# Performance work log

Measured on AMD Instinct MI355X. Metric: run time of the kernel, lower is better.

The kernel has to match this reference:

```python
import jax, jax.numpy as jnp
import numpy as np

HIDDEN = 2048
N_HEADS = 32
N_KV_HEADS = 8
HEAD_DIM = HIDDEN // N_HEADS  # 64
N_REP = N_HEADS // N_KV_HEADS  # 4
ROPE_THETA = 10000.0


def setup_inputs() -> dict:
    key = jax.random.key(0)
    ks = jax.random.split(key, 6)
    B, S = 1, 2048
    scale = 0.02
    return {
        "hidden_states": jax.random.normal(ks[0], (B, S, HIDDEN), dtype=jnp.float32),
        "Wq": jax.random.normal(ks[1], (HIDDEN, N_HEADS * HEAD_DIM), dtype=jnp.float32) * scale,
        "Wk": jax.random.normal(ks[2], (HIDDEN, N_KV_HEADS * HEAD_DIM), dtype=jnp.float32) * scale,
        "Wv": jax.random.normal(ks[3], (HIDDEN, N_KV_HEADS * HEAD_DIM), dtype=jnp.float32) * scale,
        "Wo": jax.random.normal(ks[4], (HIDDEN, HIDDEN), dtype=jnp.float32) * scale,
        "position_ids": jnp.arange(S, dtype=jnp.int64 if jax.config.jax_enable_x64 else jnp.int32)[None, :],
    }


def _rope_cos_sin(position_ids, dtype):
    # inv_freq: [head_dim//2]
    inv_freq = 1.0 / (ROPE_THETA ** (jnp.arange(0, HEAD_DIM, 2, dtype=jnp.float32) / HEAD_DIM))
    # freqs: [B, S, head_dim//2]
    freqs = position_ids.astype(jnp.float32)[:, :, None] * inv_freq[None, None, :]
    emb = jnp.concatenate([freqs, freqs], axis=-1)  # [B, S, head_dim]
    return jnp.cos(emb).astype(dtype), jnp.sin(emb).astype(dtype)


def _rotate_half(x):
    x1, x2 = jnp.split(x, 2, axis=-1)
    return jnp.concatenate([-x2, x1], axis=-1)


def reference(hidden_states, Wq, Wk, Wv, Wo, position_ids):
    B, S, _ = hidden_states.shape
    # projections -> [B, H, S, D]
    q = (hidden_states @ Wq).reshape(B, S, N_HEADS, HEAD_DIM).transpose(0, 2, 1, 3)
    k = (hidden_states @ Wk).reshape(B, S, N_KV_HEADS, HEAD_DIM).transpose(0, 2, 1, 3)
    v = (hidden_states @ Wv).reshape(B, S, N_KV_HEADS, HEAD_DIM).transpose(0, 2, 1, 3)

    cos, sin = _rope_cos_sin(position_ids, hidden_states.dtype)
    cos = cos[:, None, :, :]  # [B,1,S,D]
    sin = sin[:, None, :, :]
    q = q * cos + _rotate_half(q) * sin
    k = k * cos + _rotate_half(k) * sin

    # GQA: expand kv heads
    k = jnp.repeat(k, N_REP, axis=1)  # [B, H, S, D]
    v = jnp.repeat(v, N_REP, axis=1)

    scores = jnp.einsum("bhqd,bhkd->bhqk", q, k) / np.sqrt(HEAD_DIM).astype(np.float32)
    # additive causal mask
    causal = jnp.tril(jnp.ones((S, S), dtype=bool))
    scores = jnp.where(causal[None, None, :, :], scores, jnp.finfo(jnp.float32).min)
    attn = jax.nn.softmax(scores.astype(jnp.float32), axis=-1).astype(q.dtype)

    out = jnp.einsum("bhqk,bhkd->bhqd", attn, v)  # [B,H,S,D]
    out = out.transpose(0, 2, 1, 3).reshape(B, S, HIDDEN)
    return out @ Wo
```

## Files before the change

### kernel.cpp

```cpp
#include <hip/hip_runtime.h>
#include <stdint.h>

typedef __attribute__((ext_vector_type(8))) short short8;
typedef __attribute__((ext_vector_type(4))) float floatx4;
typedef __attribute__((ext_vector_type(16))) float floatx16;

__device__ __forceinline__ float b2f(unsigned short u) {
    union { unsigned int i; float f; } x; x.i = ((unsigned int)u) << 16; return x.f;
}
__device__ __forceinline__ unsigned short f2b(float f) {
    unsigned int x = __float_as_uint(f);
    return (unsigned short)((x + 0x7FFFu + ((x >> 16) & 1u)) >> 16);
}
__device__ __forceinline__ unsigned int cvt_pk_bf16(float lo, float hi) {
    unsigned int r;
    asm("v_cvt_pk_bf16_f32 %0, %1, %2" : "=v"(r) : "v"(lo), "v"(hi));
    return r;
}
__device__ __forceinline__ float exp2_(float x) {
    float r;
    asm("v_exp_f32 %0, %1" : "=v"(r) : "v"(x));
    return r;
}

__device__ __forceinline__ void gload_lds16(const void* g, void* l) {
    __builtin_amdgcn_global_load_lds((const __attribute__((address_space(1))) unsigned int*)g,
                                     (__attribute__((address_space(3))) unsigned int*)l, 16, 0, 0);
}

__global__ __launch_bounds__(256)
void prep_kernel(const float* __restrict__ Wq, const float* __restrict__ Wk,
                 const float* __restrict__ Wv, const float* __restrict__ Wo,
                 const float* __restrict__ hs,
                 unsigned short* __restrict__ Wqkv, unsigned short* __restrict__ WoT,
                 unsigned short* __restrict__ hs_b) {
    __shared__ float tile[64][65];
    int b = blockIdx.x;
    if (b >= 2560) {
        int i = ((b - 2560) * 256 + threadIdx.x) * 4;
        float4 v = *reinterpret_cast<const float4*>(hs + i);
        hs_b[i + 0] = f2b(v.x);
        hs_b[i + 1] = f2b(v.y);
        hs_b[i + 2] = f2b(v.z);
        hs_b[i + 3] = f2b(v.w);
        return;
    }
    const float* in;
    unsigned short* out;
    int bx, by, ld_in, ld_out;
    if (b < 1024) {
        in = Wq; out = Wqkv; bx = b & 31; by = b >> 5; ld_in = 2048; ld_out = 2048;
    } else if (b < 1280) {
        int c = b - 1024;
        in = Wk; out = Wqkv + (size_t)2048 * 2048; bx = c & 7; by = c >> 3; ld_in = 512; ld_out = 2048;
    } else if (b < 1536) {
        int c = b - 1280;
        in = Wv; out = Wqkv + (size_t)2560 * 2048; bx = c & 7; by = c >> 3; ld_in = 512; ld_out = 2048;
    } else {
        int c = b - 1536;
        in = Wo; out = WoT; bx = c & 31; by = c >> 5; ld_in = 2048; ld_out = 2048;
    }
    int tx = threadIdx.x & 63, ty = threadIdx.x >> 6;
    int c0 = bx * 64, r0 = by * 64;
    #pragma unroll
    for (int i = 0; i < 64; i += 4)
        tile[ty + i][tx] = in[(size_t)(r0 + ty + i) * ld_in + c0 + tx];
    __syncthreads();
    #pragma unroll
    for (int i = 0; i < 64; i += 4)
        out[(size_t)(c0 + ty + i) * ld_out + r0 + tx] = f2b(tile[tx][ty + i]);
}

template<int MODE>
__global__ __launch_bounds__(256)
void gemm64x128(const unsigned short* __restrict__ A, const unsigned short* __restrict__ BT,
                void* __restrict__ Cout, unsigned short* __restrict__ vTout,
                int M, int N, int K) {
    __shared__ __align__(16) unsigned short As[2][64 * 64];
    __shared__ __align__(16) unsigned short Bs[2][128 * 64];
    int tid = threadIdx.x;
    int l = tid & 63, w = tid >> 6;
    int lr = l & 15, lg = l >> 4;

    int gx = gridDim.x;
    int nwg = gx * gridDim.y;
    int flat = blockIdx.y * gx + blockIdx.x;
    int q8 = nwg >> 3;
    int f2 = (flat & 7) * q8 + (flat >> 3);
    int bx = f2 % gx, by = f2 / gx;
    int nb = bx * 128, mb = by * 64;

    floatx4 acc[4][2];
    #pragma unroll
    for (int m = 0; m < 4; ++m)
        #pragma unroll
        for (int f = 0; f < 2; ++f) acc[m][f] = (floatx4)(0.f);

    int ca1 = tid + 256;
    int ra0 = tid >> 3, ja0 = (tid & 7) ^ (ra0 & 7);
    int ra1 = ca1 >> 3, ja1 = (ca1 & 7) ^ (ra1 & 7);
    const unsigned short* Ag0 = A + (size_t)(mb + ra0) * K + ja0 * 8;
    const unsigned short* Ag1 = A + (size_t)(mb + ra1) * K + ja1 * 8;
    const unsigned short* Bg[4];
    #pragma unroll
    for (int i = 0; i < 4; ++i) {
        int c = tid + 256 * i;
        int r = c >> 3, j = (c & 7) ^ (r & 7);
        Bg[i] = BT + (size_t)(nb + r) * K + j * 8;
    }

    auto stage = [&](int buf, int kb) {
        gload_lds16(Ag0 + kb, &As[buf][tid * 8]);
        gload_lds16(Ag1 + kb, &As[buf][ca1 * 8]);
        #pragma unroll
        for (int i = 0; i < 4; ++i)
            gload_lds16(Bg[i] + kb, &Bs[buf][(tid + 256 * i) * 8]);
    };

    int nsteps = K >> 6;
    stage(0, 0);
    for (int it = 0; it < nsteps; ++it) {
        int nxt = (it + 1 < nsteps) ? it + 1 : it;
        stage((it + 1) & 1, nxt * 64);
        asm volatile("s_waitcnt vmcnt(6)" ::: "memory");
        __builtin_amdgcn_s_barrier();
        __builtin_amdgcn_sched_barrier(0);

        const unsigned short* Ab = As[it & 1];
        const unsigned short* Bb = Bs[it & 1];
        #pragma unroll
        for (int kh = 0; kh < 2; ++kh) {
            int sl = ((kh * 4 + lg) ^ (lr & 7)) * 8;
            short8 af[4], bf[2];
            #pragma unroll
            for (int m = 0; m < 4; ++m)
                af[m] = *reinterpret_cast<const short8*>(Ab + (m * 16 + lr) * 64 + sl);
            #pragma unroll
            for (int f = 0; f < 2; ++f)
                bf[f] = *reinterpret_cast<const short8*>(Bb + (w * 32 + f * 16 + lr) * 64 + sl);
            #pragma unroll
            for (int m = 0; m < 4; ++m)
                #pragma unroll
                for (int f = 0; f < 2; ++f)
                    acc[m][f] = __builtin_amdgcn_mfma_f32_16x16x32_bf16(af[m], bf[f], acc[m][f], 0, 0, 0);
        }
        __builtin_amdgcn_sched_barrier(0);
        __builtin_amdgcn_s_barrier();
    }
    asm volatile("s_waitcnt vmcnt(0)" ::: "memory");

    #pragma unroll
    for (int m = 0; m < 4; ++m) {
        int orow = mb + m * 16 + lg * 4;
        #pragma unroll
        for (int f = 0; f < 2; ++f) {
            int ocol = nb + w * 32 + f * 16 + lr;
            if (MODE == 2 && ocol >= 2560) {
                int d = ocol - 2560;
                int kvh2 = d >> 6, dd = d & 63, dh = dd >> 5, lq2 = dd & 31;
                int t64 = orow >> 6, so = orow & 63;
                int w2 = so >> 5, so32 = so & 31, kc = so32 >> 4, so16 = so32 & 15;
                int hl2 = so16 >> 3, e0 = so16 & 7;
                size_t addr = ((size_t)((kvh2 * 32 + t64) * 8) + w2 * 4 + dh * 2 + kc) * 512
                            + (hl2 * 32 + lq2) * 8 + e0;
                unsigned long long pk =
                    (unsigned long long)cvt_pk_bf16(acc[m][f][0], acc[m][f][1])
                  | ((unsigned long long)cvt_pk_bf16(acc[m][f][2], acc[m][f][3]) << 32);
                *reinterpret_cast<unsigned long long*>(vTout + addr) = pk;
            } else {
                #pragma unroll
                for (int r = 0; r < 4; ++r) {
                    if (MODE == 1)
                        ((float*)Cout)[(size_t)(orow + r) * N + ocol] = acc[m][f][r];
                    else
                        ((unsigned short*)Cout)[(size_t)(orow + r) * N + ocol] = f2b(acc[m][f][r]);
                }
            }
        }
    }
}

__global__ void rope_kernel(unsigned short* __restrict__ qkv, unsigned short* __restrict__ kB,
                            const int* __restrict__ pos_ids) {
    int idx = blockIdx.x * blockDim.x + threadIdx.x;
    int i = idx & 31;
    int hh = (idx >> 5) % 40;
    int s = idx / 1280;
    float pos = (float)pos_ids[s];
    float inv = exp2f(-0.41524101186092029f * (float)i);
    float a = pos * inv;
    float sn, cs;
    __sincosf(a, &sn, &cs);
    if (hh < 32) {
        unsigned short* p = qkv + (size_t)s * 3072 + hh * 64;
        float x1 = b2f(p[i]), x2 = b2f(p[i + 32]);
        const float scale = 0.18033688011112042f;
        p[i]      = f2b((x1 * cs - x2 * sn) * scale);
        p[i + 32] = f2b((x2 * cs + x1 * sn) * scale);
    } else {
        int kvh = hh - 32;
        const unsigned short* p = qkv + (size_t)s * 3072 + 2048 + kvh * 64;
        float x1 = b2f(p[i]), x2 = b2f(p[i + 32]);
        float r1 = x1 * cs - x2 * sn;
        float r2 = x2 * cs + x1 * sn;
        int t32 = s >> 5, lq = s & 31;
        int dc = i >> 4, hl = (i >> 3) & 1, e = i & 7;
        size_t base = (((size_t)(kvh * 64 + t32) * 4) * 64 + hl * 32 + lq) * 8 + e;
        kB[base + (size_t)dc * 512]       = f2b(r1);
        kB[base + (size_t)(dc + 2) * 512] = f2b(r2);
    }
}

__global__ __launch_bounds__(128, 2)
void attn_kernel(const unsigned short* __restrict__ QKV,
                 const unsigned short* __restrict__ KB,
                 const unsigned short* __restrict__ VB,
                 unsigned short* __restrict__ O) {
    const int LDQ = 3072, HID = 2048;
    __shared__ float Ms[64 * 36];

    int tid = threadIdx.x;
    int l = tid & 63, w = tid >> 6;
    int lq = l & 31, hl = l >> 5;
    int b = blockIdx.x;
    int h = b & 31;
    int band = 63 - (b >> 5);
    int nT = (band >> 1) + 1;
    int kvh = h >> 2;
    int qrow = band * 32 + lq;

    short8 qf[4];
    {
        const unsigned short* Qr = QKV + (size_t)qrow * LDQ + h * 64;
        #pragma unroll
        for (int c = 0; c < 4; ++c)
            qf[c] = *reinterpret_cast<const short8*>(Qr + c * 16 + hl * 8);
    }

    const unsigned short* Kp = KB + ((size_t)(kvh * 64 + w) * 4) * 512 + l * 8;
    const size_t KSTEP = 2 * 4 * 512;
    const unsigned short* Vbase = VB + ((size_t)kvh * 32 * 8 + (size_t)w * 4) * 512 + l * 8;

    floatx16 acc[2];
    acc[0] = (floatx16)(0.f); acc[1] = (floatx16)(0.f);
    float m_run = -1e30f, l_run = 0.f;

    auto process = [&](const short8* kf, int c0w, bool diag,
                       short8 v00, short8 v01, short8 v10, short8 v11) {
        floatx16 st = (floatx16)(0.f);
        __builtin_amdgcn_s_setprio(1);
        #pragma unroll
        for (int dc = 0; dc < 4; ++dc)
            st = __builtin_amdgcn_mfma_f32_32x32x16_bf16(kf[dc], qf[dc], st, 0, 0, 0);
        __builtin_amdgcn_s_setprio(0);
        if (diag) {
            #pragma unroll
            for (int r = 0; r < 16; ++r) {
                int key = c0w + (r & 3) + 8 * (r >> 2) + 4 * hl;
                if (key > qrow) st[r] = -1e30f;
            }
        }
        float t0 = fmaxf(fmaxf(st[0], st[1]), fmaxf(st[2], st[3]));
        float t1 = fmaxf(fmaxf(st[4], st[5]), fmaxf(st[6], st[7]));
        float t2 = fmaxf(fmaxf(st[8], st[9]), fmaxf(st[10], st[11]));
        float t3 = fmaxf(fmaxf(st[12], st[13]), fmaxf(st[14], st[15]));
        float tm = fmaxf(fmaxf(t0, t1), fmaxf(t2, t3));
        tm = fmaxf(tm, __shfl_xor(tm, 32));
        if (!__all(tm <= m_run + 11.5f)) {
            float mn = fmaxf(m_run, tm);
            float al = exp2_(m_run - mn);
            l_run *= al;
            acc[0] *= al;
            acc[1] *= al;
            m_run = mn;
        }
        float p[16];
        #pragma unroll
        for (int r = 0; r < 16; ++r) p[r] = exp2_(st[r] - m_run);
        float s0 = (p[0] + p[1]) + (p[2] + p[3]);
        float s1 = (p[4] + p[5]) + (p[6] + p[7]);
        float s2 = (p[8] + p[9]) + (p[10] + p[11]);
        float s3 = (p[12] + p[13]) + (p[14] + p[15]);
        float rs = (s0 + s1) + (s2 + s3);
        rs += __shfl_xor(rs, 32);
        l_run += rs;
        unsigned int u[4][2];
        #pragma unroll
        for (int B2 = 0; B2 < 4; ++B2) {
            u[B2][0] = cvt_pk_bf16(p[B2 * 4 + 0], p[B2 * 4 + 1]);
            u[B2][1] = cvt_pk_bf16(p[B2 * 4 + 2], p[B2 * 4 + 3]);
        }
        asm volatile("s_waitcnt vmcnt(4)" ::: "memory");
        __builtin_amdgcn_sched_barrier(0);
        #pragma unroll
        for (int kc = 0; kc < 2; ++kc) {
            unsigned int o0 = u[2 * kc][0],     o1 = u[2 * kc][1];
            unsigned int e0 = u[2 * kc + 1][0], e1 = u[2 * kc + 1][1];
            unsigned int t0x = (unsigned int)__shfl((int)o0, l ^ 32);
            unsigned int t1x = (unsigned int)__shfl((int)o1, l ^ 32);
            unsigned int s0p = (unsigned int)__shfl((int)e0, l ^ 32);
            unsigned int s1p = (unsigned int)__shfl((int)e1, l ^ 32);
            union { unsigned int uu[4]; short8 s8; } pf;
            pf.uu[0] = hl ? s0p : o0;
            pf.uu[1] = hl ? s1p : o1;
            pf.uu[2] = hl ? e0 : t0x;
            pf.uu[3] = hl ? e1 : t1x;
            __builtin_amdgcn_s_setprio(1);
            acc[0] = __builtin_amdgcn_mfma_f32_32x32x16_bf16(kc ? v01 : v00, pf.s8, acc[0], 0, 0, 0);
            acc[1] = __builtin_amdgcn_mfma_f32_32x32x16_bf16(kc ? v11 : v10, pf.s8, acc[1], 0, 0, 0);
            __builtin_amdgcn_s_setprio(0);
        }
    };

    short8 kA[4], kBr[4];
    #pragma unroll
    for (int dc = 0; dc < 4; ++dc)
        kA[dc] = *reinterpret_cast<const short8*>(Kp + dc * 512);

    int j = 0;
    while (true) {
        {
            bool last = (j == nT - 1);
            const unsigned short* Vs = Vbase + (size_t)j * 8 * 512;
            short8 v00 = *reinterpret_cast<const short8*>(Vs);
            short8 v01 = *reinterpret_cast<const short8*>(Vs + 512);
            short8 v10 = *reinterpret_cast<const short8*>(Vs + 1024);
            short8 v11 = *reinterpret_cast<const short8*>(Vs + 1536);
            __builtin_amdgcn_sched_barrier(0);
            const unsigned short* Kn = last ? Kp : Kp + KSTEP;
            #pragma unroll
            for (int dc = 0; dc < 4; ++dc)
                kBr[dc] = *reinterpret_cast<const short8*>(Kn + dc * 512);
            asm volatile("s_waitcnt vmcnt(8)" ::: "memory");
            __builtin_amdgcn_sched_barrier(0);
            process(kA, j * 64 + w * 32, last, v00, v01, v10, v11);
            if (last) break;
            ++j; Kp = Kn;
        }
        {
            bool last = (j == nT - 1);
            const unsigned short* Vs = Vbase + (size_t)j * 8 * 512;
            short8 v00 = *reinterpret_cast<const short8*>(Vs);
            short8 v01 = *reinterpret_cast<const short8*>(Vs + 512);
            short8 v10 = *reinterpret_cast<const short8*>(Vs + 1024);
            short8 v11 = *reinterpret_cast<const short8*>(Vs + 1536);
            __builtin_amdgcn_sched_barrier(0);
            const unsigned short* Kn = last ? Kp : Kp + KSTEP;
            #pragma unroll
            for (int dc = 0; dc < 4; ++dc)
                kA[dc] = *reinterpret_cast<const short8*>(Kn + dc * 512);
            asm volatile("s_waitcnt vmcnt(8)" ::: "memory");
            __builtin_amdgcn_sched_barrier(0);
            process(kBr, j * 64 + w * 32, last, v00, v01, v10, v11);
            if (last) break;
            ++j; Kp = Kn;
        }
    }
    asm volatile("s_waitcnt vmcnt(0)" ::: "memory");
    __syncthreads();

    if (w == 1) {
        Ms[l * 36 + 0] = m_run;
        Ms[l * 36 + 1] = l_run;
        #pragma unroll
        for (int d = 0; d < 2; ++d)
            #pragma unroll
            for (int r = 0; r < 16; ++r)
                Ms[l * 36 + 2 + d * 16 + r] = acc[d][r];
    }
    __syncthreads();
    if (w == 0) {
        float m1 = Ms[l * 36 + 0], l1 = Ms[l * 36 + 1];
        float mm = fmaxf(m_run, m1);
        float a0 = exp2_(m_run - mm), a1 = exp2_(m1 - mm);
        float inv = 1.0f / (l_run * a0 + l1 * a1);
        a0 *= inv; a1 *= inv;
        unsigned short* Op = O + (size_t)qrow * HID + h * 64 + hl * 4;
        #pragma unroll
        for (int d = 0; d < 2; ++d)
            #pragma unroll
            for (int g4 = 0; g4 < 4; ++g4) {
                float v0 = acc[d][g4 * 4 + 0] * a0 + Ms[l * 36 + 2 + d * 16 + g4 * 4 + 0] * a1;
                float v1 = acc[d][g4 * 4 + 1] * a0 + Ms[l * 36 + 2 + d * 16 + g4 * 4 + 1] * a1;
                float v2 = acc[d][g4 * 4 + 2] * a0 + Ms[l * 36 + 2 + d * 16 + g4 * 4 + 2] * a1;
                float v3 = acc[d][g4 * 4 + 3] * a0 + Ms[l * 36 + 2 + d * 16 + g4 * 4 + 3] * a1;
                unsigned long long pk = (unsigned long long)cvt_pk_bf16(v0, v1)
                                      | ((unsigned long long)cvt_pk_bf16(v2, v3) << 32);
                *reinterpret_cast<unsigned long long*>(Op + d * 32 + g4 * 8) = pk;
            }
    }
}

extern "C" void kernel_launch(void* const* d_in, const int* in_sizes, int n_in,
                              void* d_out, int out_size, void* d_ws, size_t ws_size,
                              hipStream_t stream) {
    const int S = 2048, HID = 2048, KVD = 512, NQKV = 3072;
    const float* hs = (const float*)d_in[0];
    const float* Wq = (const float*)d_in[1];
    const float* Wk = (const float*)d_in[2];
    const float* Wv = (const float*)d_in[3];
    const float* Wo = (const float*)d_in[4];
    const int* pos  = (const int*)d_in[5];

    char* base = (char*)d_ws;
    auto alloc = [&](size_t bytes) {
        char* r = base;
        base += (bytes + 255) & ~(size_t)255;
        return r;
    };
    unsigned short* hs_b     = (unsigned short*)alloc((size_t)S * HID * 2);
    unsigned short* Wqkv     = (unsigned short*)alloc((size_t)NQKV * HID * 2);
    unsigned short* WoT      = (unsigned short*)alloc((size_t)HID * HID * 2);
    unsigned short* qkv      = (unsigned short*)alloc((size_t)S * NQKV * 2);
    unsigned short* vB       = (unsigned short*)alloc((size_t)KVD * S * 2);
    unsigned short* kBuf     = (unsigned short*)alloc((size_t)KVD * S * 2);
    unsigned short* attn_out = (unsigned short*)alloc((size_t)S * HID * 2);

    prep_kernel<<<6656, 256, 0, stream>>>(Wq, Wk, Wv, Wo, hs, Wqkv, WoT, hs_b);

    gemm64x128<2><<<dim3(NQKV / 128, S / 64), 256, 0, stream>>>(hs_b, Wqkv, qkv, vB, S, NQKV, HID);

    rope_kernel<<<10240, 256, 0, stream>>>(qkv, kBuf, pos);

    attn_kernel<<<2048, 128, 0, stream>>>(qkv, kBuf, vB, attn_out);

    gemm64x128<1><<<dim3(HID / 128, S / 64), 256, 0, stream>>>(attn_out, WoT, (float*)d_out, nullptr, S, HID, HID);
}
```

Baseline: 125.8 us.

## Fuse RoPE into QKV projection GEMM epilogue via LDS exchange

Result: faster. 121.6 us, median of 2 (-3.3%).

```diff
diff --git a/kernel.cpp b/kernel.cpp
--- a/kernel.cpp
+++ b/kernel.cpp
@@ -75,6 +75,7 @@
 __global__ __launch_bounds__(256)
 void gemm64x128(const unsigned short* __restrict__ A, const unsigned short* __restrict__ BT,
                 void* __restrict__ Cout, unsigned short* __restrict__ vTout,
+                unsigned short* __restrict__ kBout, const int* __restrict__ pos_ids,
                 int M, int N, int K) {
     __shared__ __align__(16) unsigned short As[2][64 * 64];
     __shared__ __align__(16) unsigned short Bs[2][128 * 64];
@@ -149,13 +150,69 @@
     }
     asm volatile("s_waitcnt vmcnt(0)" ::: "memory");
 
+    if (MODE == 2 && nb < 2560) {
+        float* Xs = (float*)&Bs[0][0];
+        if (w & 1) {
+            float* dst = Xs + ((size_t)(w >> 1) * 64 + l) * 32;
+            #pragma unroll
+            for (int m = 0; m < 4; ++m)
+                #pragma unroll
+                for (int f = 0; f < 2; ++f)
+                    #pragma unroll
+                    for (int r = 0; r < 4; ++r)
+                        dst[m * 8 + f * 4 + r] = acc[m][f][r];
+        }
+        __syncthreads();
+        if (!(w & 1)) {
+            const float* src = Xs + ((size_t)(w >> 1) * 64 + l) * 32;
+            bool isQ = (nb < 2048);
+            float qs = isQ ? 0.18033688011112042f : 1.0f;
+            int kvh = isQ ? 0 : (((nb - 2048) >> 6) + (w >> 1));
+            #pragma unroll
+            for (int f = 0; f < 2; ++f) {
+                int i = f * 16 + lr;
+                float invf = exp2f(-0.41524101186092029f * (float)i);
+                int ocol = nb + w * 32 + f * 16 + lr;
+                #pragma unroll
+                for (int m = 0; m < 4; ++m) {
+                    int orow = mb + m * 16 + lg * 4;
+                    #pragma unroll
+                    for (int r = 0; r < 4; ++r) {
+                        int s = orow + r;
+                        float pos = (float)pos_ids[s];
+                        float sn, cs;
+                        __sincosf(pos * invf, &sn, &cs);
+                        float x1 = acc[m][f][r];
+                        float x2 = src[m * 8 + f * 4 + r];
+                        float r1 = (x1 * cs - x2 * sn) * qs;
+                        float r2 = (x2 * cs + x1 * sn) * qs;
+                        if (isQ) {
+                            unsigned short* C = (unsigned short*)Cout;
+                            C[(size_t)s * N + ocol]      = f2b(r1);
+                            C[(size_t)s * N + ocol + 32] = f2b(r2);
+                        } else {
+                            int t32 = s >> 5, lq2 = s & 31;
+                            int d1 = i, d2 = i + 32;
+                            int dc1 = d1 >> 4, hl1 = (d1 >> 3) & 1, e1 = d1 & 7;
+                            int dc2 = d2 >> 4, hl2 = (d2 >> 3) & 1, e2 = d2 & 7;
+                            size_t tb = (size_t)(kvh * 64 + t32) * 2048;
+                            kBout[tb + (size_t)dc1 * 512 + (hl1 * 32 + lq2) * 8 + e1] = f2b(r1);
+                            kBout[tb + (size_t)dc2 * 512 + (hl2 * 32 + lq2) * 8 + e2] = f2b(r2);
+                        }
+                    }
+                }
+            }
+        }
+        return;
+    }
+
     #pragma unroll
     for (int m = 0; m < 4; ++m) {
         int orow = mb + m * 16 + lg * 4;
         #pragma unroll
         for (int f = 0; f < 2; ++f) {
             int ocol = nb + w * 32 + f * 16 + lr;
-            if (MODE == 2 && ocol >= 2560) {
+            if (MODE == 2) {
                 int d = ocol - 2560;
                 int kvh2 = d >> 6, dd = d & 63, dh = dd >> 5, lq2 = dd & 31;
                 int t64 = orow >> 6, so = orow & 63;
@@ -180,37 +237,6 @@
     }
 }
 
-__global__ void rope_kernel(unsigned short* __restrict__ qkv, unsigned short* __restrict__ kB,
-                            const int* __restrict__ pos_ids) {
-    int idx = blockIdx.x * blockDim.x + threadIdx.x;
-    int i = idx & 31;
-    int hh = (idx >> 5) % 40;
-    int s = idx / 1280;
-    float pos = (float)pos_ids[s];
-    float inv = exp2f(-0.41524101186092029f * (float)i);
-    float a = pos * inv;
-    float sn, cs;
-    __sincosf(a, &sn, &cs);
-    if (hh < 32) {
-        unsigned short* p = qkv + (size_t)s * 3072 + hh * 64;
-        float x1 = b2f(p[i]), x2 = b2f(p[i + 32]);
-        const float scale = 0.18033688011112042f;
-        p[i]      = f2b((x1 * cs - x2 * sn) * scale);
-        p[i + 32] = f2b((x2 * cs + x1 * sn) * scale);
-    } else {
-        int kvh = hh - 32;
-        const unsigned short* p = qkv + (size_t)s * 3072 + 2048 + kvh * 64;
-        float x1 = b2f(p[i]), x2 = b2f(p[i + 32]);
-        float r1 = x1 * cs - x2 * sn;
-        float r2 = x2 * cs + x1 * sn;
-        int t32 = s >> 5, lq = s & 31;
-        int dc = i >> 4, hl = (i >> 3) & 1, e = i & 7;
-        size_t base = (((size_t)(kvh * 64 + t32) * 4) * 64 + hl * 32 + lq) * 8 + e;
-        kB[base + (size_t)dc * 512]       = f2b(r1);
-        kB[base + (size_t)(dc + 2) * 512] = f2b(r2);
-    }
-}
-
 __global__ __launch_bounds__(128, 2)
 void attn_kernel(const unsigned short* __restrict__ QKV,
                  const unsigned short* __restrict__ KB,
@@ -418,11 +444,9 @@
 
     prep_kernel<<<6656, 256, 0, stream>>>(Wq, Wk, Wv, Wo, hs, Wqkv, WoT, hs_b);
 
-    gemm64x128<2><<<dim3(NQKV / 128, S / 64), 256, 0, stream>>>(hs_b, Wqkv, qkv, vB, S, NQKV, HID);
-
-    rope_kernel<<<10240, 256, 0, stream>>>(qkv, kBuf, pos);
+    gemm64x128<2><<<dim3(NQKV / 128, S / 64), 256, 0, stream>>>(hs_b, Wqkv, qkv, vB, kBuf, pos, S, NQKV, HID);
 
     attn_kernel<<<2048, 128, 0, stream>>>(qkv, kBuf, vB, attn_out);
 
-    gemm64x128<1><<<dim3(HID / 128, S / 64), 256, 0, stream>>>(attn_out, WoT, (float*)d_out, nullptr, S, HID, HID);
-}
+    gemm64x128<1><<<dim3(HID / 128, S / 64), 256, 0, stream>>>(attn_out, WoT, (float*)d_out, nullptr, nullptr, nullptr, S, HID, HID);
+}
```
